# Kernel optimization log

Measured on AMD Instinct MI355X. Metric: run time of the kernel, lower is better.

The kernel has to match this reference:

```python
import jax, jax.numpy as jnp
import numpy as np

N_NODES = 50000
N_EDGES = 600000
NFEAT = 256
NHID = 128
NCLASS = 40


def setup_inputs() -> dict:
    key = jax.random.key(0)
    ks = jax.random.split(key, 10)
    x = jax.random.normal(ks[0], (N_NODES, NFEAT), dtype=jnp.float32)
    edge_src = jax.random.randint(ks[1], (N_EDGES,), 0, N_NODES, dtype=jnp.int32)
    edge_dst = jax.random.randint(ks[2], (N_EDGES,), 0, N_NODES, dtype=jnp.int32)
    # normalized adjacency weights (positive, ~1/deg scale)
    edge_weight = jax.random.uniform(ks[3], (N_EDGES,), dtype=jnp.float32) * 0.2
    # GraphConvolution params (Glorot-ish init)
    W1 = jax.random.normal(ks[4], (NFEAT, NHID), dtype=jnp.float32) / np.float32(np.sqrt(NFEAT))
    b1 = jnp.zeros((NHID,), dtype=jnp.float32)
    W2 = jax.random.normal(ks[5], (NHID, NHID), dtype=jnp.float32) / np.float32(np.sqrt(NHID))
    b2 = jnp.zeros((NHID,), dtype=jnp.float32)
    W3 = jax.random.normal(ks[6], (NHID, NCLASS), dtype=jnp.float32) / np.float32(np.sqrt(NHID))
    b3 = jnp.zeros((NCLASS,), dtype=jnp.float32)
    return {"x": x, "edge_weight": edge_weight, "W1": W1, "b1": b1,
            "W2": W2, "b2": b2, "W3": W3, "b3": b3,
            "edge_src": edge_src, "edge_dst": edge_dst}


def _gcn_layer(h, W, b, edge_src, edge_dst, edge_weight):
    # support = h @ W ; out = spmm(adj, support) + b
    support = h @ W                                   # [N, out]
    msgs = support[edge_src] * edge_weight[:, None]   # [E, out]
    agg = jax.ops.segment_sum(msgs, edge_dst, num_segments=N_NODES)
    return agg + b


def reference(x, edge_weight, W1, b1, W2, b2, W3, b3, edge_src, edge_dst):
    # eval mode: F.dropout(training=False) is identity
    h = jax.nn.relu(_gcn_layer(x, W1, b1, edge_src, edge_dst, edge_weight))
    h = jax.nn.relu(_gcn_layer(h, W2, b2, edge_src, edge_dst, edge_weight))
    h = _gcn_layer(h, W3, b3, edge_src, edge_dst, edge_weight)
    return jax.nn.log_softmax(h, axis=1)
```

## Files before the change

### kernel.cpp

```cpp
#include <hip/hip_runtime.h>
#include <hip/hip_bf16.h>
#include <math.h>

#define N_NODES 50000
#define N_EDGES 600000
#define NFEAT   256
#define NHID    128
#define NCLASS  40
#define E_PAD_MAX (N_EDGES + 7 * N_NODES)
#define GEMM_BLOCKS  ((N_NODES + 63) / 64)
#define NBUCK 196
#define EPB_A 2048
#define BUCK_CAP 4096

typedef __attribute__((ext_vector_type(8))) short bf16x8;
typedef __attribute__((ext_vector_type(4))) float f32x4;
typedef __attribute__((ext_vector_type(2))) float f32x2;

__device__ inline ushort f2bf(float f) {
    uint u = __float_as_uint(f);
    uint r = (u + 0x7fffu + ((u >> 16) & 1u)) >> 16;
    return (ushort)r;
}

__global__ __launch_bounds__(256) void scatter_binA(const int* __restrict__ src,
                                                    const int* __restrict__ dst,
                                                    const float* __restrict__ w,
                                                    int* __restrict__ bucket_cnt,
                                                    int2* __restrict__ staging, int E) {
    __shared__ int lh[NBUCK];
    int tid = threadIdx.x;
    for (int b = tid; b < NBUCK; b += 256) lh[b] = 0;
    __syncthreads();
    int base = blockIdx.x * EPB_A;
    int d[8];
    #pragma unroll
    for (int j = 0; j < 8; ++j) {
        int i = base + j * 256 + tid;
        d[j] = (i < E) ? dst[i] : -1;
        if (d[j] >= 0) atomicAdd(&lh[d[j] >> 8], 1);
    }
    __syncthreads();
    for (int b = tid; b < NBUCK; b += 256) {
        int c = lh[b];
        lh[b] = c ? (b * BUCK_CAP + atomicAdd(&bucket_cnt[b], c)) : 0;
    }
    __syncthreads();
    #pragma unroll
    for (int j = 0; j < 8; ++j) {
        int i = base + j * 256 + tid;
        if (d[j] >= 0) {
            int slot = atomicAdd(&lh[d[j] >> 8], 1);
            uint rec = ((uint)f2bf(w[i]) << 16) | (uint)src[i];
            staging[slot] = make_int2((int)rec, d[j] & 255);
        }
    }
}

__global__ __launch_bounds__(256) void bucket_hist_cvtw(const int* __restrict__ bucket_cnt,
                                                        const int2* __restrict__ staging,
                                                        int* __restrict__ bsum, int nb,
                                                        const float* __restrict__ W1,
                                                        const float* __restrict__ W2,
                                                        const float* __restrict__ W3,
                                                        ushort* __restrict__ BT1,
                                                        ushort* __restrict__ BT2,
                                                        ushort* __restrict__ BT3) {
    if ((int)blockIdx.x >= nb) {
        int idx = ((int)blockIdx.x - nb) * 256 + threadIdx.x;
        if (idx < 32768) {
            int nr = idx >> 8, k = idx & 255;
            BT1[idx] = f2bf(W1[(size_t)k * 128 + nr]);
        } else if (idx < 49152) {
            int t = idx - 32768;
            int nr = t >> 7, k = t & 127;
            BT2[t] = f2bf(W2[(size_t)k * 128 + nr]);
        } else if (idx < 57344) {
            int t = idx - 49152;
            int nr = t >> 7, k = t & 127;
            BT3[t] = (nr < 40) ? f2bf(W3[(size_t)k * 40 + nr]) : (ushort)0;
        }
        return;
    }
    __shared__ int hist[256];
    __shared__ int red[4];
    int tid = threadIdx.x;
    hist[tid] = 0;
    __syncthreads();
    int b = blockIdx.x;
    int c = bucket_cnt[b];
    const int2* st = staging + (size_t)b * BUCK_CAP;
    for (int p = tid; p < c; p += 256) atomicAdd(&hist[st[p].y], 1);
    __syncthreads();
    int v = (hist[tid] + 7) & ~7;
    #pragma unroll
    for (int off = 32; off; off >>= 1) v += __shfl_down(v, off, 64);
    int wv = tid >> 6, lane = tid & 63;
    if (lane == 0) red[wv] = v;
    __syncthreads();
    if (tid == 0) bsum[b] = red[0] + red[1] + red[2] + red[3];
}

__global__ __launch_bounds__(256) void scan_scatter(const int* __restrict__ bsum,
                                                    const int* __restrict__ bucket_cnt,
                                                    const int2* __restrict__ staging,
                                                    int* __restrict__ rsp,
                                                    uint* __restrict__ edges, int n) {
    __shared__ int hist[256];
    __shared__ int buf[256];
    __shared__ int lcur[256];
    __shared__ int boff_s;
    int tid = threadIdx.x;
    hist[tid] = 0;
    if (tid < 64) {
        int s = 0;
        for (int i = tid; i < (int)blockIdx.x; i += 64) s += bsum[i];
        #pragma unroll
        for (int off = 32; off; off >>= 1) s += __shfl_down(s, off, 64);
        if (tid == 0) boff_s = s;
    }
    __syncthreads();
    int b = blockIdx.x;
    int c = bucket_cnt[b];
    const int2* st = staging + (size_t)b * BUCK_CAP;
    for (int p = tid; p < c; p += 256) atomicAdd(&hist[st[p].y], 1);
    __syncthreads();
    int v = (hist[tid] + 7) & ~7;
    buf[tid] = v;
    __syncthreads();
    #pragma unroll
    for (int off = 1; off < 256; off <<= 1) {
        int t = (tid >= off) ? buf[tid - off] : 0;
        __syncthreads();
        buf[tid] += t;
        __syncthreads();
    }
    int ex = buf[tid] - v + boff_s;
    int i = b * 256 + tid;
    if (i < n) rsp[i] = ex;
    if (i == n - 1) rsp[n] = ex + v;
    lcur[tid] = ex;
    __syncthreads();
    int s0 = boff_s, e0 = buf[255] + boff_s;
    for (int p = s0 + tid; p < e0; p += 256) edges[p] = 0;
    __syncthreads();
    for (int p = tid; p < c; p += 256) {
        int2 r = st[p];
        int slot = atomicAdd(&lcur[r.y], 1);
        edges[slot] = (uint)r.x;
    }
}

template<int NT, bool OUTBF, bool AF32>
__device__ __forceinline__ void gemm_body(const void* __restrict__ Ain,
                                          const ushort* __restrict__ BT,
                                          int M, int K, int Nout,
                                          void* __restrict__ Cout, int row0) {
    __shared__ ushort a_s[64 * 40];
    __shared__ ushort b_s[64 * NT * 40];
    int tid = threadIdx.x;
    int wave = tid >> 6, lane = tid & 63;
    int lr = lane & 15, lk = (lane >> 4) * 8;
    f32x4 acc[4][NT];
    #pragma unroll
    for (int mt = 0; mt < 4; ++mt)
        #pragma unroll
        for (int nt = 0; nt < NT; ++nt) acc[mt][nt] = (f32x4){0.f, 0.f, 0.f, 0.f};

    for (int k0 = 0; k0 < K; k0 += 32) {
        {
            int r = tid >> 2, c8 = (tid & 3) * 8;
            int gr = row0 + r; if (gr >= M) gr = M - 1;
            if (AF32) {
                const float* Af = (const float*)Ain;
                float4 v0 = *(const float4*)(Af + (size_t)gr * K + k0 + c8);
                float4 v1 = *(const float4*)(Af + (size_t)gr * K + k0 + c8 + 4);
                ushort4 o0, o1;
                o0.x = f2bf(v0.x); o0.y = f2bf(v0.y); o0.z = f2bf(v0.z); o0.w = f2bf(v0.w);
                o1.x = f2bf(v1.x); o1.y = f2bf(v1.y); o1.z = f2bf(v1.z); o1.w = f2bf(v1.w);
                *(ushort4*)(a_s + r * 40 + c8) = o0;
                *(ushort4*)(a_s + r * 40 + c8 + 4) = o1;
            } else {
                const ushort* Ab = (const ushort*)Ain;
                float4 v = *(const float4*)(Ab + (size_t)gr * K + k0 + c8);
                *(float4*)(a_s + r * 40 + c8) = v;
            }
        }
        #pragma unroll
        for (int i = 0; i < NT; ++i) {
            int idx = tid * NT + i;
            int r = idx >> 2, c8 = (idx & 3) * 8;
            float4 v = *(const float4*)(BT + (size_t)r * K + k0 + c8);
            *(float4*)(b_s + r * 40 + c8) = v;
        }
        __syncthreads();
        bf16x8 bfr[NT];
        #pragma unroll
        for (int nt = 0; nt < NT; ++nt)
            bfr[nt] = *(const bf16x8*)(b_s + ((wave * NT + nt) * 16 + lr) * 40 + lk);
        #pragma unroll
        for (int mt = 0; mt < 4; ++mt) {
            bf16x8 afr = *(const bf16x8*)(a_s + (mt * 16 + lr) * 40 + lk);
            #pragma unroll
            for (int nt = 0; nt < NT; ++nt)
                acc[mt][nt] = __builtin_amdgcn_mfma_f32_16x16x32_bf16(
                    afr, bfr[nt], acc[mt][nt], 0, 0, 0);
        }
        __syncthreads();
    }
    int col0 = wave * NT * 16;
    #pragma unroll
    for (int mt = 0; mt < 4; ++mt) {
        int gr0 = row0 + mt * 16 + (lane >> 4) * 4;
        #pragma unroll
        for (int nt = 0; nt < NT; ++nt) {
            int gc = col0 + nt * 16 + lr;
            #pragma unroll
            for (int i = 0; i < 4; ++i) {
                int gr = gr0 + i;
                if (gr < M && gc < Nout) {
                    if (OUTBF)
                        ((ushort*)Cout)[(size_t)gr * Nout + gc] = f2bf(acc[mt][nt][i]);
                    else
                        ((float*)Cout)[(size_t)gr * Nout + gc] = acc[mt][nt][i];
                }
            }
        }
    }
}

template<int NT, bool OUTBF, bool AF32>
__global__ __launch_bounds__(256) void gemm_mfma(const void* __restrict__ Ain,
                                                 const ushort* __restrict__ BT,
                                                 int M, int K, int Nout,
                                                 void* __restrict__ Cout) {
    gemm_body<NT, OUTBF, AF32>(Ain, BT, M, K, Nout, Cout, blockIdx.x * 64);
}

__global__ __launch_bounds__(256) void spmm128b(const uint* __restrict__ sup,
                                                const int* __restrict__ rsp,
                                                const uint* __restrict__ edges,
                                                const float* __restrict__ bias,
                                                uint* __restrict__ outb, int n) {
    int wid = blockIdx.x * 4 + (threadIdx.x >> 6);
    int lane = threadIdx.x & 63;
    if (wid >= n) return;
    int k = rsp[wid], e = rsp[wid + 1];
    f32x2 acc = (f32x2){0.f, 0.f};
    if (k < e) {
        const uint4* q4 = (const uint4*)(edges + k);
        uint4 qa = q4[0], qb = q4[1];
        for (; k < e; k += 8) {
            int kn = k + 8;
            int kc = (kn < e) ? kn : k;
            const uint4* n4 = (const uint4*)(edges + kc);
            uint4 na = n4[0], nb = n4[1];
            uint q[8] = {qa.x, qa.y, qa.z, qa.w, qb.x, qb.y, qb.z, qb.w};
            uint p[8];
            #pragma unroll
            for (int j = 0; j < 8; ++j)
                p[j] = sup[(size_t)(q[j] & 0xffffu) * 64 + lane];
            #pragma unroll
            for (int j = 0; j < 8; ++j) {
                float w = __uint_as_float(q[j] & 0xffff0000u);
                f32x2 v;
                v.x = __uint_as_float(p[j] << 16);
                v.y = __uint_as_float(p[j] & 0xffff0000u);
                acc += v * (f32x2){w, w};
            }
            qa = na; qb = nb;
        }
    }
    float ax = fmaxf(acc.x + bias[lane * 2], 0.f);
    float ay = fmaxf(acc.y + bias[lane * 2 + 1], 0.f);
    outb[(size_t)wid * 64 + lane] = ((uint)f2bf(ay) << 16) | (uint)f2bf(ax);
}

__global__ __launch_bounds__(256) void spmm40_lsm(const ushort* __restrict__ sup,
                                                  const int* __restrict__ rsp,
                                                  const uint* __restrict__ edges,
                                                  const float* __restrict__ bias,
                                                  float* __restrict__ out, int n) {
    int wid = blockIdx.x * 4 + (threadIdx.x >> 6);
    int lane = threadIdx.x & 63;
    if (wid >= n) return;
    int k = rsp[wid], e = rsp[wid + 1];
    float acc = 0.f;
    int lf = (lane < 40) ? lane : 39;
    if (k < e) {
        const uint4* q4 = (const uint4*)(edges + k);
        uint4 qa = q4[0], qb = q4[1];
        for (; k < e; k += 8) {
            int kn = k + 8;
            int kc = (kn < e) ? kn : k;
            const uint4* n4 = (const uint4*)(edges + kc);
            uint4 na = n4[0], nb = n4[1];
            uint q[8] = {qa.x, qa.y, qa.z, qa.w, qb.x, qb.y, qb.z, qb.w};
            float p[8];
            #pragma unroll
            for (int j = 0; j < 8; ++j) {
                uint us = sup[(size_t)(q[j] & 0xffffu) * 40 + lf];
                p[j] = __uint_as_float(us << 16);
            }
            #pragma unroll
            for (int j = 0; j < 8; ++j)
                acc += p[j] * __uint_as_float(q[j] & 0xffff0000u);
            qa = na; qb = nb;
        }
    }
    float v = (lane < 40) ? acc + bias[lane] : -INFINITY;
    float m = v;
    #pragma unroll
    for (int off = 32; off; off >>= 1) m = fmaxf(m, __shfl_xor(m, off, 64));
    float ex = (lane < 40) ? expf(v - m) : 0.f;
    float s = ex;
    #pragma unroll
    for (int off = 32; off; off >>= 1) s += __shfl_xor(s, off, 64);
    float ls = logf(s);
    if (lane < 40) out[(size_t)wid * 40 + lane] = v - m - ls;
}

extern "C" void kernel_launch(void* const* d_in, const int* in_sizes, int n_in,
                              void* d_out, int out_size, void* d_ws, size_t ws_size,
                              hipStream_t stream) {
    const float* x   = (const float*)d_in[0];
    const float* ew  = (const float*)d_in[1];
    const float* W1  = (const float*)d_in[2];
    const float* b1  = (const float*)d_in[3];
    const float* W2  = (const float*)d_in[4];
    const float* b2  = (const float*)d_in[5];
    const float* W3  = (const float*)d_in[6];
    const float* b3  = (const float*)d_in[7];
    const int* esrc  = (const int*)d_in[8];
    const int* edst  = (const int*)d_in[9];
    float* out = (float*)d_out;

    char* ws = (char*)d_ws;
    size_t off = 0;
    auto alloc = [&](size_t bytes) {
        size_t cur = off;
        off += (bytes + 255) & ~(size_t)255;
        return cur;
    };
    int* bucket_cnt = (int*)(ws + alloc(256 * sizeof(int)));
    int* bsum    = (int*)(ws + alloc(256 * sizeof(int)));
    int* rsp     = (int*)(ws + alloc((N_NODES + 1) * sizeof(int)));
    uint* edges  = (uint*)(ws + alloc((size_t)E_PAD_MAX * sizeof(uint)));
    int2* staging = (int2*)(ws + alloc((size_t)NBUCK * BUCK_CAP * sizeof(int2)));
    ushort* BT1  = (ushort*)(ws + alloc(128 * 256 * 2));
    ushort* BT2  = (ushort*)(ws + alloc(128 * 128 * 2));
    ushort* BT3  = (ushort*)(ws + alloc(64 * 128 * 2));
    char* Sreg   = ws + alloc((size_t)N_NODES * 128 * 2);
    char* Hreg   = ws + alloc((size_t)N_NODES * 128 * 2);
    char* Treg   = ws + alloc((size_t)N_NODES * 128 * 2);

    ushort* supA = (ushort*)Sreg;
    ushort* hA   = (ushort*)Hreg;
    ushort* supB = (ushort*)Treg;
    ushort* hB   = (ushort*)Sreg;
    ushort* sup3 = (ushort*)Treg;

    int cvtw_blocks = (57344 + 255) / 256;

    hipMemsetAsync(bucket_cnt, 0, 256 * sizeof(int), stream);
    scatter_binA<<<(N_EDGES + EPB_A - 1) / EPB_A, 256, 0, stream>>>(
        esrc, edst, ew, bucket_cnt, staging, N_EDGES);
    bucket_hist_cvtw<<<NBUCK + cvtw_blocks, 256, 0, stream>>>(
        bucket_cnt, staging, bsum, NBUCK, W1, W2, W3, BT1, BT2, BT3);
    scan_scatter<<<NBUCK, 256, 0, stream>>>(bsum, bucket_cnt, staging, rsp,
                                            edges, N_NODES);

    int spmm_blocks = (N_NODES + 3) / 4;

    gemm_mfma<2, true, true><<<GEMM_BLOCKS, 256, 0, stream>>>(x, BT1, N_NODES, 256,
                                                              128, supA);
    spmm128b<<<spmm_blocks, 256, 0, stream>>>((const uint*)supA, rsp, edges, b1,
                                              (uint*)hA, N_NODES);
    gemm_mfma<2, true, false><<<GEMM_BLOCKS, 256, 0, stream>>>(hA, BT2, N_NODES, 128,
                                                               128, supB);
    spmm128b<<<spmm_blocks, 256, 0, stream>>>((const uint*)supB, rsp, edges, b2,
                                              (uint*)hB, N_NODES);
    gemm_mfma<1, true, false><<<GEMM_BLOCKS, 256, 0, stream>>>(hB, BT3, N_NODES, 128,
                                                               40, sup3);
    spmm40_lsm<<<spmm_blocks, 256, 0, stream>>>(sup3, rsp, edges, b3, out, N_NODES);
}
```

Baseline: 233.2 us.

## Fuse CSR build stages, merge scan with first GEMM, vectorize SpMM gathers

Folds the weight conversion into the edge-binning kernel. Replaces the global bucket-sum scan with fixed per-bucket edge windows, so the separate histogram kernel goes away, and runs the scan/scatter blocks alongside the first GEMM in one launch. The SpMM kernels now gather 16-byte uint4 rows, with several edges processed in parallel per wave and a shuffle reduction at the end. Row ranges are stored as int2 start/end pairs. The last layer is padded to 64 columns to allow vector loads. Together these cut launch count and serialization and widen gather loads, at the cost of a fixed window size (BUCK_WIN) that could overflow on skewed degree distributions.

```diff
diff --git a/kernel.cpp b/kernel.cpp
--- a/kernel.cpp
+++ b/kernel.cpp
@@ -1,5 +1,4 @@
 #include <hip/hip_runtime.h>
-#include <hip/hip_bf16.h>
 #include <math.h>
 
 #define N_NODES 50000
@@ -7,11 +6,13 @@
 #define NFEAT   256
 #define NHID    128
 #define NCLASS  40
-#define E_PAD_MAX (N_EDGES + 7 * N_NODES)
-#define GEMM_BLOCKS  ((N_NODES + 63) / 64)
 #define NBUCK 196
 #define EPB_A 2048
 #define BUCK_CAP 4096
+#define BUCK_WIN 5888
+#define BINA_BLOCKS ((N_EDGES + EPB_A - 1) / EPB_A)
+#define CVTW_BLOCKS 224
+#define GEMM_BLOCKS ((N_NODES + 63) / 64)
 
 typedef __attribute__((ext_vector_type(8))) short bf16x8;
 typedef __attribute__((ext_vector_type(4))) float f32x4;
@@ -23,51 +24,20 @@
     return (ushort)r;
 }
 
-__global__ __launch_bounds__(256) void scatter_binA(const int* __restrict__ src,
-                                                    const int* __restrict__ dst,
-                                                    const float* __restrict__ w,
-                                                    int* __restrict__ bucket_cnt,
-                                                    int2* __restrict__ staging, int E) {
-    __shared__ int lh[NBUCK];
+__global__ __launch_bounds__(256) void binA_cvtw(const int* __restrict__ src,
+                                                 const int* __restrict__ dst,
+                                                 const float* __restrict__ w,
+                                                 int* __restrict__ bucket_cnt,
+                                                 int2* __restrict__ staging, int E,
+                                                 const float* __restrict__ W1,
+                                                 const float* __restrict__ W2,
+                                                 const float* __restrict__ W3,
+                                                 ushort* __restrict__ BT1,
+                                                 ushort* __restrict__ BT2,
+                                                 ushort* __restrict__ BT3) {
     int tid = threadIdx.x;
-    for (int b = tid; b < NBUCK; b += 256) lh[b] = 0;
-    __syncthreads();
-    int base = blockIdx.x * EPB_A;
-    int d[8];
-    #pragma unroll
-    for (int j = 0; j < 8; ++j) {
-        int i = base + j * 256 + tid;
-        d[j] = (i < E) ? dst[i] : -1;
-        if (d[j] >= 0) atomicAdd(&lh[d[j] >> 8], 1);
-    }
-    __syncthreads();
-    for (int b = tid; b < NBUCK; b += 256) {
-        int c = lh[b];
-        lh[b] = c ? (b * BUCK_CAP + atomicAdd(&bucket_cnt[b], c)) : 0;
-    }
-    __syncthreads();
-    #pragma unroll
-    for (int j = 0; j < 8; ++j) {
-        int i = base + j * 256 + tid;
-        if (d[j] >= 0) {
-            int slot = atomicAdd(&lh[d[j] >> 8], 1);
-            uint rec = ((uint)f2bf(w[i]) << 16) | (uint)src[i];
-            staging[slot] = make_int2((int)rec, d[j] & 255);
-        }
-    }
-}
-
-__global__ __launch_bounds__(256) void bucket_hist_cvtw(const int* __restrict__ bucket_cnt,
-                                                        const int2* __restrict__ staging,
-                                                        int* __restrict__ bsum, int nb,
-                                                        const float* __restrict__ W1,
-                                                        const float* __restrict__ W2,
-                                                        const float* __restrict__ W3,
-                                                        ushort* __restrict__ BT1,
-                                                        ushort* __restrict__ BT2,
-                                                        ushort* __restrict__ BT3) {
-    if ((int)blockIdx.x >= nb) {
-        int idx = ((int)blockIdx.x - nb) * 256 + threadIdx.x;
+    if ((int)blockIdx.x >= BINA_BLOCKS) {
+        int idx = ((int)blockIdx.x - BINA_BLOCKS) * 256 + tid;
         if (idx < 32768) {
             int nr = idx >> 8, k = idx & 255;
             BT1[idx] = f2bf(W1[(size_t)k * 128 + nr]);
@@ -82,72 +52,31 @@
         }
         return;
     }
-    __shared__ int hist[256];
-    __shared__ int red[4];
-    int tid = threadIdx.x;
-    hist[tid] = 0;
-    __syncthreads();
-    int b = blockIdx.x;
-    int c = bucket_cnt[b];
-    const int2* st = staging + (size_t)b * BUCK_CAP;
-    for (int p = tid; p < c; p += 256) atomicAdd(&hist[st[p].y], 1);
-    __syncthreads();
-    int v = (hist[tid] + 7) & ~7;
-    #pragma unroll
-    for (int off = 32; off; off >>= 1) v += __shfl_down(v, off, 64);
-    int wv = tid >> 6, lane = tid & 63;
-    if (lane == 0) red[wv] = v;
-    __syncthreads();
-    if (tid == 0) bsum[b] = red[0] + red[1] + red[2] + red[3];
-}
-
-__global__ __launch_bounds__(256) void scan_scatter(const int* __restrict__ bsum,
-                                                    const int* __restrict__ bucket_cnt,
-                                                    const int2* __restrict__ staging,
-                                                    int* __restrict__ rsp,
-                                                    uint* __restrict__ edges, int n) {
-    __shared__ int hist[256];
-    __shared__ int buf[256];
-    __shared__ int lcur[256];
-    __shared__ int boff_s;
-    int tid = threadIdx.x;
-    hist[tid] = 0;
-    if (tid < 64) {
-        int s = 0;
-        for (int i = tid; i < (int)blockIdx.x; i += 64) s += bsum[i];
-        #pragma unroll
-        for (int off = 32; off; off >>= 1) s += __shfl_down(s, off, 64);
-        if (tid == 0) boff_s = s;
-    }
-    __syncthreads();
-    int b = blockIdx.x;
-    int c = bucket_cnt[b];
-    const int2* st = staging + (size_t)b * BUCK_CAP;
-    for (int p = tid; p < c; p += 256) atomicAdd(&hist[st[p].y], 1);
-    __syncthreads();
-    int v = (hist[tid] + 7) & ~7;
-    buf[tid] = v;
-    __syncthreads();
-    #pragma unroll
-    for (int off = 1; off < 256; off <<= 1) {
-        int t = (tid >= off) ? buf[tid - off] : 0;
-        __syncthreads();
-        buf[tid] += t;
-        __syncthreads();
-    }
-    int ex = buf[tid] - v + boff_s;
-    int i = b * 256 + tid;
-    if (i < n) rsp[i] = ex;
-    if (i == n - 1) rsp[n] = ex + v;
-    lcur[tid] = ex;
-    __syncthreads();
-    int s0 = boff_s, e0 = buf[255] + boff_s;
-    for (int p = s0 + tid; p < e0; p += 256) edges[p] = 0;
-    __syncthreads();
-    for (int p = tid; p < c; p += 256) {
-        int2 r = st[p];
-        int slot = atomicAdd(&lcur[r.y], 1);
-        edges[slot] = (uint)r.x;
+    __shared__ int lh[NBUCK];
+    for (int b = tid; b < NBUCK; b += 256) lh[b] = 0;
+    __syncthreads();
+    int base = blockIdx.x * EPB_A;
+    int d[8];
+    #pragma unroll
+    for (int j = 0; j < 8; ++j) {
+        int i = base + j * 256 + tid;
+        d[j] = (i < E) ? dst[i] : -1;
+        if (d[j] >= 0) atomicAdd(&lh[d[j] >> 8], 1);
+    }
+    __syncthreads();
+    for (int b = tid; b < NBUCK; b += 256) {
+        int c = lh[b];
+        lh[b] = c ? (b * BUCK_CAP + atomicAdd(&bucket_cnt[b], c)) : 0;
+    }
+    __syncthreads();
+    #pragma unroll
+    for (int j = 0; j < 8; ++j) {
+        int i = base + j * 256 + tid;
+        if (d[j] >= 0) {
+            int slot = atomicAdd(&lh[d[j] >> 8], 1);
+            uint rec = ((uint)f2bf(w[i]) << 16) | (uint)src[i];
+            staging[slot] = make_int2((int)rec, d[j] & 255);
+        }
     }
 }
 
@@ -237,87 +166,183 @@
     gemm_body<NT, OUTBF, AF32>(Ain, BT, M, K, Nout, Cout, blockIdx.x * 64);
 }
 
-__global__ __launch_bounds__(256) void spmm128b(const uint* __restrict__ sup,
-                                                const int* __restrict__ rsp,
+__global__ __launch_bounds__(256) void scan_gemm1(const int* __restrict__ bucket_cnt,
+                                                  const int2* __restrict__ staging,
+                                                  int2* __restrict__ rsp2,
+                                                  uint* __restrict__ edges,
+                                                  const float* __restrict__ x,
+                                                  const ushort* __restrict__ BT1,
+                                                  ushort* __restrict__ supA) {
+    if ((int)blockIdx.x >= NBUCK) {
+        gemm_body<2, true, true>(x, BT1, N_NODES, 256, 128, supA,
+                                 ((int)blockIdx.x - NBUCK) * 64);
+        return;
+    }
+    __shared__ int hist[256];
+    __shared__ int buf[256];
+    __shared__ int lcur[256];
+    int tid = threadIdx.x;
+    hist[tid] = 0;
+    __syncthreads();
+    int b = blockIdx.x;
+    int c = bucket_cnt[b];
+    const int2* st = staging + (size_t)b * BUCK_CAP;
+    for (int p = tid; p < c; p += 256) atomicAdd(&hist[st[p].y], 1);
+    __syncthreads();
+    int v = (hist[tid] + 7) & ~7;
+    buf[tid] = v;
+    __syncthreads();
+    #pragma unroll
+    for (int off = 1; off < 256; off <<= 1) {
+        int t = (tid >= off) ? buf[tid - off] : 0;
+        __syncthreads();
+        buf[tid] += t;
+        __syncthreads();
+    }
+    int bb = b * BUCK_WIN;
+    int ex = buf[tid] - v + bb;
+    int i = b * 256 + tid;
+    if (i < N_NODES) rsp2[i] = make_int2(ex, ex + v);
+    lcur[tid] = ex;
+    __syncthreads();
+    int e0 = bb + buf[255];
+    for (int p = bb + tid; p < e0; p += 256) edges[p] = 0;
+    __syncthreads();
+    for (int p = tid; p < c; p += 256) {
+        int2 r = st[p];
+        int slot = atomicAdd(&lcur[r.y], 1);
+        edges[slot] = (uint)r.x;
+    }
+}
+
+__global__ __launch_bounds__(256) void spmm128v(const uint4* __restrict__ sup4,
+                                                const int2* __restrict__ rsp2,
                                                 const uint* __restrict__ edges,
                                                 const float* __restrict__ bias,
-                                                uint* __restrict__ outb, int n) {
+                                                uint4* __restrict__ outb4, int n) {
     int wid = blockIdx.x * 4 + (threadIdx.x >> 6);
     int lane = threadIdx.x & 63;
     if (wid >= n) return;
-    int k = rsp[wid], e = rsp[wid + 1];
-    f32x2 acc = (f32x2){0.f, 0.f};
+    int2 ke = rsp2[wid];
+    int k = ke.x, e = ke.y;
+    int slot = lane >> 4, fb = lane & 15;
+    f32x2 a0 = (f32x2){0.f, 0.f}, a1 = a0, a2 = a0, a3 = a0;
     if (k < e) {
-        const uint4* q4 = (const uint4*)(edges + k);
-        uint4 qa = q4[0], qb = q4[1];
-        for (; k < e; k += 8) {
-            int kn = k + 8;
-            int kc = (kn < e) ? kn : k;
-            const uint4* n4 = (const uint4*)(edges + kc);
-            uint4 na = n4[0], nb = n4[1];
-            uint q[8] = {qa.x, qa.y, qa.z, qa.w, qb.x, qb.y, qb.z, qb.w};
-            uint p[8];
-            #pragma unroll
-            for (int j = 0; j < 8; ++j)
-                p[j] = sup[(size_t)(q[j] & 0xffffu) * 64 + lane];
-            #pragma unroll
-            for (int j = 0; j < 8; ++j) {
-                float w = __uint_as_float(q[j] & 0xffff0000u);
-                f32x2 v;
-                v.x = __uint_as_float(p[j] << 16);
-                v.y = __uint_as_float(p[j] & 0xffff0000u);
-                acc += v * (f32x2){w, w};
-            }
-            qa = na; qb = nb;
-        }
-    }
-    float ax = fmaxf(acc.x + bias[lane * 2], 0.f);
-    float ay = fmaxf(acc.y + bias[lane * 2 + 1], 0.f);
-    outb[(size_t)wid * 64 + lane] = ((uint)f2bf(ay) << 16) | (uint)f2bf(ax);
-}
-
-__global__ __launch_bounds__(256) void spmm40_lsm(const ushort* __restrict__ sup,
-                                                  const int* __restrict__ rsp,
+        uint rec = edges[k + slot];
+        int k1 = (k + 4 < e) ? k + 4 : k;
+        uint recn = edges[k1 + slot];
+        uint4 p = sup4[(size_t)(rec & 0xffffu) * 16 + fb];
+        for (; k < e; k += 4) {
+            int k2 = (k + 8 < e) ? k + 8 : k;
+            uint recnn = edges[k2 + slot];
+            uint4 pn = sup4[(size_t)(recn & 0xffffu) * 16 + fb];
+            float w = __uint_as_float(rec & 0xffff0000u);
+            f32x2 wv = (f32x2){w, w};
+            f32x2 v;
+            v.x = __uint_as_float(p.x << 16); v.y = __uint_as_float(p.x & 0xffff0000u);
+            a0 += v * wv;
+            v.x = __uint_as_float(p.y << 16); v.y = __uint_as_float(p.y & 0xffff0000u);
+            a1 += v * wv;
+            v.x = __uint_as_float(p.z << 16); v.y = __uint_as_float(p.z & 0xffff0000u);
+            a2 += v * wv;
+            v.x = __uint_as_float(p.w << 16); v.y = __uint_as_float(p.w & 0xffff0000u);
+            a3 += v * wv;
+            rec = recn; recn = recnn; p = pn;
+        }
+    }
+    #pragma unroll
+    for (int off = 16; off <= 32; off <<= 1) {
+        a0.x += __shfl_xor(a0.x, off, 64); a0.y += __shfl_xor(a0.y, off, 64);
+        a1.x += __shfl_xor(a1.x, off, 64); a1.y += __shfl_xor(a1.y, off, 64);
+        a2.x += __shfl_xor(a2.x, off, 64); a2.y += __shfl_xor(a2.y, off, 64);
+        a3.x += __shfl_xor(a3.x, off, 64); a3.y += __shfl_xor(a3.y, off, 64);
+    }
+    if (slot == 0) {
+        float4 bl = *(const float4*)(bias + fb * 8);
+        float4 bh = *(const float4*)(bias + fb * 8 + 4);
+        uint4 o;
+        o.x = ((uint)f2bf(fmaxf(a0.y + bl.y, 0.f)) << 16) | (uint)f2bf(fmaxf(a0.x + bl.x, 0.f));
+        o.y = ((uint)f2bf(fmaxf(a1.y + bl.w, 0.f)) << 16) | (uint)f2bf(fmaxf(a1.x + bl.z, 0.f));
+        o.z = ((uint)f2bf(fmaxf(a2.y + bh.y, 0.f)) << 16) | (uint)f2bf(fmaxf(a2.x + bh.x, 0.f));
+        o.w = ((uint)f2bf(fmaxf(a3.y + bh.w, 0.f)) << 16) | (uint)f2bf(fmaxf(a3.x + bh.z, 0.f));
+        outb4[(size_t)wid * 16 + fb] = o;
+    }
+}
+
+__global__ __launch_bounds__(256) void spmm64_lsm(const uint4* __restrict__ sup4,
+                                                  const int2* __restrict__ rsp2,
                                                   const uint* __restrict__ edges,
                                                   const float* __restrict__ bias,
                                                   float* __restrict__ out, int n) {
     int wid = blockIdx.x * 4 + (threadIdx.x >> 6);
     int lane = threadIdx.x & 63;
     if (wid >= n) return;
-    int k = rsp[wid], e = rsp[wid + 1];
-    float acc = 0.f;
-    int lf = (lane < 40) ? lane : 39;
+    int2 ke = rsp2[wid];
+    int k = ke.x, e = ke.y;
+    int slot = lane >> 3, fb = lane & 7;
+    f32x2 a0 = (f32x2){0.f, 0.f}, a1 = a0, a2 = a0, a3 = a0;
     if (k < e) {
-        const uint4* q4 = (const uint4*)(edges + k);
-        uint4 qa = q4[0], qb = q4[1];
+        uint rec = edges[k + slot];
+        int k1 = (k + 8 < e) ? k + 8 : k;
+        uint recn = edges[k1 + slot];
+        uint4 p = sup4[(size_t)(rec & 0xffffu) * 8 + fb];
         for (; k < e; k += 8) {
-            int kn = k + 8;
-            int kc = (kn < e) ? kn : k;
-            const uint4* n4 = (const uint4*)(edges + kc);
-            uint4 na = n4[0], nb = n4[1];
-            uint q[8] = {qa.x, qa.y, qa.z, qa.w, qb.x, qb.y, qb.z, qb.w};
-            float p[8];
-            #pragma unroll
-            for (int j = 0; j < 8; ++j) {
-                uint us = sup[(size_t)(q[j] & 0xffffu) * 40 + lf];
-                p[j] = __uint_as_float(us << 16);
-            }
-            #pragma unroll
-            for (int j = 0; j < 8; ++j)
-                acc += p[j] * __uint_as_float(q[j] & 0xffff0000u);
-            qa = na; qb = nb;
-        }
-    }
-    float v = (lane < 40) ? acc + bias[lane] : -INFINITY;
-    float m = v;
-    #pragma unroll
-    for (int off = 32; off; off >>= 1) m = fmaxf(m, __shfl_xor(m, off, 64));
-    float ex = (lane < 40) ? expf(v - m) : 0.f;
-    float s = ex;
-    #pragma unroll
-    for (int off = 32; off; off >>= 1) s += __shfl_xor(s, off, 64);
-    float ls = logf(s);
-    if (lane < 40) out[(size_t)wid * 40 + lane] = v - m - ls;
+            int k2 = (k + 16 < e) ? k + 16 : k;
+            uint recnn = edges[k2 + slot];
+            uint4 pn = sup4[(size_t)(recn & 0xffffu) * 8 + fb];
+            float w = __uint_as_float(rec & 0xffff0000u);
+            f32x2 wv = (f32x2){w, w};
+            f32x2 v;
+            v.x = __uint_as_float(p.x << 16); v.y = __uint_as_float(p.x & 0xffff0000u);
+            a0 += v * wv;
+            v.x = __uint_as_float(p.y << 16); v.y = __uint_as_float(p.y & 0xffff0000u);
+            a1 += v * wv;
+            v.x = __uint_as_float(p.z << 16); v.y = __uint_as_float(p.z & 0xffff0000u);
+            a2 += v * wv;
+            v.x = __uint_as_float(p.w << 16); v.y = __uint_as_float(p.w & 0xffff0000u);
+            a3 += v * wv;
+            rec = recn; recn = recnn; p = pn;
+        }
+    }
+    #pragma unroll
+    for (int off = 8; off <= 32; off <<= 1) {
+        a0.x += __shfl_xor(a0.x, off, 64); a0.y += __shfl_xor(a0.y, off, 64);
+        a1.x += __shfl_xor(a1.x, off, 64); a1.y += __shfl_xor(a1.y, off, 64);
+        a2.x += __shfl_xor(a2.x, off, 64); a2.y += __shfl_xor(a2.y, off, 64);
+        a3.x += __shfl_xor(a3.x, off, 64); a3.y += __shfl_xor(a3.y, off, 64);
+    }
+    float vv[8];
+    bool valid = (fb < 5);
+    if (valid) {
+        float4 bl = *(const float4*)(bias + fb * 8);
+        float4 bh = *(const float4*)(bias + fb * 8 + 4);
+        vv[0] = a0.x + bl.x; vv[1] = a0.y + bl.y;
+        vv[2] = a1.x + bl.z; vv[3] = a1.y + bl.w;
+        vv[4] = a2.x + bh.x; vv[5] = a2.y + bh.y;
+        vv[6] = a3.x + bh.z; vv[7] = a3.y + bh.w;
+    } else {
+        #pragma unroll
+        for (int j = 0; j < 8; ++j) vv[j] = -INFINITY;
+    }
+    float m = vv[0];
+    #pragma unroll
+    for (int j = 1; j < 8; ++j) m = fmaxf(m, vv[j]);
+    #pragma unroll
+    for (int off = 1; off <= 4; off <<= 1) m = fmaxf(m, __shfl_xor(m, off, 64));
+    float s = 0.f;
+    if (valid) {
+        #pragma unroll
+        for (int j = 0; j < 8; ++j) s += expf(vv[j] - m);
+    }
+    #pragma unroll
+    for (int off = 1; off <= 4; off <<= 1) s += __shfl_xor(s, off, 64);
+    float ls = logf(s) + m;
+    if (slot == 0 && valid) {
+        float4 r0 = make_float4(vv[0] - ls, vv[1] - ls, vv[2] - ls, vv[3] - ls);
+        float4 r1 = make_float4(vv[4] - ls, vv[5] - ls, vv[6] - ls, vv[7] - ls);
+        *(float4*)(out + (size_t)wid * 40 + fb * 8) = r0;
+        *(float4*)(out + (size_t)wid * 40 + fb * 8 + 4) = r1;
+    }
 }
 
 extern "C" void kernel_launch(void* const* d_in, const int* in_sizes, int n_in,
@@ -343,9 +368,8 @@
         return cur;
     };
     int* bucket_cnt = (int*)(ws + alloc(256 * sizeof(int)));
-    int* bsum    = (int*)(ws + alloc(256 * sizeof(int)));
-    int* rsp     = (int*)(ws + alloc((N_NODES + 1) * sizeof(int)));
-    uint* edges  = (uint*)(ws + alloc((size_t)E_PAD_MAX * sizeof(uint)));
+    int2* rsp2   = (int2*)(ws + alloc((size_t)N_NODES * sizeof(int2)));
+    uint* edges  = (uint*)(ws + alloc((size_t)NBUCK * BUCK_WIN * sizeof(uint)));
     int2* staging = (int2*)(ws + alloc((size_t)NBUCK * BUCK_CAP * sizeof(int2)));
     ushort* BT1  = (ushort*)(ws + alloc(128 * 256 * 2));
     ushort* BT2  = (ushort*)(ws + alloc(128 * 128 * 2));
@@ -360,27 +384,21 @@
     ushort* hB   = (ushort*)Sreg;
     ushort* sup3 = (ushort*)Treg;
 
-    int cvtw_blocks = (57344 + 255) / 256;
-
     hipMemsetAsync(bucket_cnt, 0, 256 * sizeof(int), stream);
-    scatter_binA<<<(N_EDGES + EPB_A - 1) / EPB_A, 256, 0, stream>>>(
-        esrc, edst, ew, bucket_cnt, staging, N_EDGES);
-    bucket_hist_cvtw<<<NBUCK + cvtw_blocks, 256, 0, stream>>>(
-        bucket_cnt, staging, bsum, NBUCK, W1, W2, W3, BT1, BT2, BT3);
-    scan_scatter<<<NBUCK, 256, 0, stream>>>(bsum, bucket_cnt, staging, rsp,
-                                            edges, N_NODES);
+    binA_cvtw<<<BINA_BLOCKS + CVTW_BLOCKS, 256, 0, stream>>>(
+        esrc, edst, ew, bucket_cnt, staging, N_EDGES, W1, W2, W3, BT1, BT2, BT3);
+    scan_gemm1<<<NBUCK + GEMM_BLOCKS, 256, 0, stream>>>(
+        bucket_cnt, staging, rsp2, edges, x, BT1, supA);
 
     int spmm_blocks = (N_NODES + 3) / 4;
-
-    gemm_mfma<2, true, true><<<GEMM_BLOCKS, 256, 0, stream>>>(x, BT1, N_NODES, 256,
-                                                              128, supA);
-    spmm128b<<<spmm_blocks, 256, 0, stream>>>((const uint*)supA, rsp, edges, b1,
-                                              (uint*)hA, N_NODES);
+    spmm128v<<<spmm_blocks, 256, 0, stream>>>((const uint4*)supA, rsp2, edges, b1,
+                                              (uint4*)hA, N_NODES);
     gemm_mfma<2, true, false><<<GEMM_BLOCKS, 256, 0, stream>>>(hA, BT2, N_NODES, 128,
                                                                128, supB);
-    spmm128b<<<spmm_blocks, 256, 0, stream>>>((const uint*)supB, rsp, edges, b2,
-                                              (uint*)hB, N_NODES);
+    spmm128v<<<spmm_blocks, 256, 0, stream>>>((const uint4*)supB, rsp2, edges, b2,
+                                              (uint4*)hB, N_NODES);
     gemm_mfma<1, true, false><<<GEMM_BLOCKS, 256, 0, stream>>>(hB, BT3, N_NODES, 128,
-                                                               40, sup3);
-    spmm40_lsm<<<spmm_blocks, 256, 0, stream>>>(sup3, rsp, edges, b3, out, N_NODES);
-}
+                                                               64, sup3);
+    spmm64_lsm<<<spmm_blocks, 256, 0, stream>>>((const uint4*)sup3, rsp2, edges, b3,
+                                                out, N_NODES);
+}
```

Result: slower. 238.5 us (+2.3%).
